# Performance work log

Hardware: AMD Instinct MI355X
Metric: run time of the kernel (lower is better)

## Reference

```python
import jax, jax.numpy as jnp
import numpy as np

B, L, E, H, V, NC = 64, 256, 300, 128, 50000, 2
NH1, F1 = 8, 8  # GAT layer 1: 8 heads x 8 features; layer 2: 1 head x 1 feature
LRELU = 0.2


def _lstm_dir(x, W, U, b):
    # x: [B, L, E]; W: [4H, E]; U: [4H, H]; b: [4H] (b_ih + b_hh fused)
    Bq, Hq = x.shape[0], U.shape[1]
    def step(carry, xt):
        h, c = carry
        g = xt @ W.T + h @ U.T + b
        i, f, gg, o = jnp.split(g, 4, axis=-1)  # PyTorch gate order i,f,g,o
        c = jax.nn.sigmoid(f) * c + jax.nn.sigmoid(i) * jnp.tanh(gg)
        h = jax.nn.sigmoid(o) * jnp.tanh(c)
        return (h, c), h
    h0 = jnp.zeros((Bq, Hq), x.dtype)
    _, hs = jax.lax.scan(step, (h0, h0), jnp.swapaxes(x, 0, 1))
    return jnp.swapaxes(hs, 0, 1)  # [B, L, H]


def bilstm(x, Wf, Uf, bf, Wb, Ub, bb):
    hf = _lstm_dir(x, Wf, Uf, bf)
    hb = _lstm_dir(x[:, ::-1], Wb, Ub, bb)[:, ::-1]
    return jnp.concatenate([hf, hb], axis=-1)  # [B, L, 2H]


def gat_layer(x, W, a_src, a_trg, bias, n_heads, f_out, concat, elu_act):
    # Dense equivalent of GAT IMP3 on a fully-connected graph (edge (s,t): src=s, trg=t).
    Bq, Lq, _ = x.shape
    proj = (x @ W.T).reshape(Bq, Lq, n_heads, f_out)        # [B,L,NH,F]
    s_src = jnp.einsum('blhf,hf->blh', proj, a_src)          # [B,L,NH]
    s_trg = jnp.einsum('blhf,hf->blh', proj, a_trg)
    sc = jax.nn.leaky_relu(s_src[:, :, None, :] + s_trg[:, None, :, :], LRELU)  # [B,S,T,NH]
    m = jnp.max(sc, axis=(1, 2, 3), keepdims=True)           # global max per graph (as in IMP3)
    e = jnp.exp(sc - m)
    A = e / (jnp.sum(e, axis=1, keepdims=True) + 1e-16)      # softmax over sources per target
    out = jnp.einsum('bsth,bshf->bthf', A, proj)             # scatter-aggregate to targets
    if concat:
        out = out.reshape(Bq, Lq, n_heads * f_out)
    else:
        out = out.mean(axis=2)
    out = out + bias
    if elu_act:
        out = jax.nn.elu(out)
    return out, A


def setup_inputs() -> dict:
    key = jax.random.key(0)
    ks = jax.random.split(key, 20)
    n = lambda k, shape, s=0.05: (jax.random.normal(k, shape, jnp.float32) * s)
    return {
        'input_ids': jax.random.randint(ks[0], (B, L), 0, V, jnp.int32),
        'attention_mask': jnp.ones((B, L), bool),
        'emb': n(ks[1], (V, E), 0.1),
        'Wih_f': n(ks[2], (4 * H, E)), 'Whh_f': n(ks[3], (4 * H, H)), 'b_f': jnp.zeros((4 * H,), jnp.float32),
        'Wih_b': n(ks[4], (4 * H, E)), 'Whh_b': n(ks[5], (4 * H, H)), 'b_b': jnp.zeros((4 * H,), jnp.float32),
        'g1_W': n(ks[6], (NH1 * F1, 2 * H)), 'g1_src': n(ks[7], (NH1, F1), 0.1), 'g1_trg': n(ks[8], (NH1, F1), 0.1), 'g1_b': jnp.zeros((NH1 * F1,), jnp.float32),
        'g2_W': n(ks[9], (1, NH1 * F1)), 'g2_src': n(ks[10], (1, 1), 0.1), 'g2_trg': n(ks[11], (1, 1), 0.1), 'g2_b': jnp.zeros((1,), jnp.float32),
        'ctx': n(ks[12], (L, 1), 0.1),
        'lin_W': n(ks[13], (B, 2 * H)), 'lin_b': jnp.zeros((B,), jnp.float32),
        'out_W': n(ks[14], (NC, B)), 'out_b': jnp.zeros((NC,), jnp.float32),
    }


def reference(input_ids, attention_mask, emb, Wih_f, Whh_f, b_f, Wih_b, Whh_b, b_b,
              g1_W, g1_src, g1_trg, g1_b, g2_W, g2_src, g2_trg, g2_b,
              ctx, lin_W, lin_b, out_W, out_b):
    x = emb[input_ids]                                   # [B,L,E] (dropout = eval no-op)
    h_seq = bilstm(x, Wih_f, Whh_f, b_f, Wih_b, Whh_b, b_b)  # [B,L,2H]
    h1, _ = gat_layer(h_seq, g1_W, g1_src, g1_trg, g1_b, NH1, F1, True, True)
    _, A2 = gat_layer(h1, g2_W, g2_src, g2_trg, g2_b, 1, 1, False, False)
    att2 = A2[..., 0]                                    # [B, src, trg] == att.view(-1, 2H) rows
    att = jnp.einsum('bst,t->bs', att2, ctx[:, 0])       # mm with context_vector
    att = jnp.where(attention_mask, att, -jnp.inf)
    att = jax.nn.softmax(att, axis=1)                    # [B,L]
    pooled = jnp.max(h_seq * att[..., None], axis=1)     # [B,2H]
    hcl = jax.nn.relu(pooled @ lin_W.T + lin_b)
    logits = hcl @ out_W.T + out_b                       # [B,NC]
    return (logits, att)
```

## Files before the change

### kernel.cpp

```cpp
#include <hip/hip_runtime.h>
#include <math.h>
#include <stdint.h>

#define Bq 64
#define Lq 256
#define Eq 300
#define Hq 128
#define MQ (Bq*Lq)
#define AST 320

#define LRELU_S 0.2f

__device__ __forceinline__ float lrelu(float x) { return x > 0.f ? x : LRELU_S * x; }

typedef short short8 __attribute__((ext_vector_type(8)));
typedef float f32x4v __attribute__((ext_vector_type(4)));

__device__ __forceinline__ unsigned short f2bf(float x) {
  unsigned u = __float_as_uint(x);
  u += 0x7FFFu + ((u >> 16) & 1u);
  return (unsigned short)(u >> 16);
}
__device__ __forceinline__ float bf2f(unsigned short h) {
  return __uint_as_float(((unsigned)h) << 16);
}

__global__ __launch_bounds__(256) void gather_conv_kernel(
    const float* __restrict__ emb, const int* __restrict__ ids,
    unsigned short* __restrict__ Agh, unsigned short* __restrict__ Agl)
{
  const int JOBS = MQ * 80;
  for (int j = blockIdx.x * blockDim.x + threadIdx.x; j < JOBS;
       j += gridDim.x * blockDim.x) {
    int row = j / 80, c = j - row * 80;
    uint2 ph = make_uint2(0u, 0u), pl = make_uint2(0u, 0u);
    if (c < 75) {
      float4 v = *(const float4*)(emb + (size_t)ids[row] * Eq + c * 4);
      unsigned short h0 = f2bf(v.x), h1 = f2bf(v.y), h2 = f2bf(v.z), h3 = f2bf(v.w);
      unsigned short l0 = f2bf(v.x - bf2f(h0)), l1 = f2bf(v.y - bf2f(h1));
      unsigned short l2 = f2bf(v.z - bf2f(h2)), l3 = f2bf(v.w - bf2f(h3));
      ph.x = (unsigned)h0 | ((unsigned)h1 << 16); ph.y = (unsigned)h2 | ((unsigned)h3 << 16);
      pl.x = (unsigned)l0 | ((unsigned)l1 << 16); pl.y = (unsigned)l2 | ((unsigned)l3 << 16);
    }
    size_t off = (size_t)row * AST + c * 4;
    *(uint2*)(Agh + off) = ph;
    *(uint2*)(Agl + off) = pl;
  }
}

#define BM 64
#define BN 64
#define BK 16

__global__ __launch_bounds__(256) void gemm_awt(
    const float* __restrict__ Asrc, const int* __restrict__ ids,
    const float* __restrict__ W, const float* __restrict__ bias,
    float* __restrict__ C, int M, int N, int K)
{
  __shared__ float As[BK][BM + 4];
  __shared__ float Bs[BK][BN + 4];
  int tid = threadIdx.x;
  int tx = tid & 15, ty = tid >> 4;
  int row0 = blockIdx.x * BM, col0 = blockIdx.y * BN;

  int lrow = tid >> 2;
  int lk   = (tid & 3) << 2;

  const float* Arow;
  {
    int r = row0 + lrow;
    int id = ids ? ids[r] : r;
    Arow = Asrc + (size_t)id * K;
  }
  const float* Wrow = W + (size_t)(col0 + lrow) * K;

  float acc[4][4] = {};

  for (int k0 = 0; k0 < K; k0 += BK) {
    int kk = k0 + lk;
    float4 av, bv;
    if (kk + 3 < K) {
      av = *(const float4*)(Arow + kk);
      bv = *(const float4*)(Wrow + kk);
    } else {
      float a0 = (kk + 0 < K) ? Arow[kk + 0] : 0.f;
      float a1 = (kk + 1 < K) ? Arow[kk + 1] : 0.f;
      float a2 = (kk + 2 < K) ? Arow[kk + 2] : 0.f;
      float a3 = (kk + 3 < K) ? Arow[kk + 3] : 0.f;
      av = make_float4(a0, a1, a2, a3);
      float b0 = (kk + 0 < K) ? Wrow[kk + 0] : 0.f;
      float b1 = (kk + 1 < K) ? Wrow[kk + 1] : 0.f;
      float b2 = (kk + 2 < K) ? Wrow[kk + 2] : 0.f;
      float b3 = (kk + 3 < K) ? Wrow[kk + 3] : 0.f;
      bv = make_float4(b0, b1, b2, b3);
    }
    As[lk + 0][lrow] = av.x; As[lk + 1][lrow] = av.y;
    As[lk + 2][lrow] = av.z; As[lk + 3][lrow] = av.w;
    Bs[lk + 0][lrow] = bv.x; Bs[lk + 1][lrow] = bv.y;
    Bs[lk + 2][lrow] = bv.z; Bs[lk + 3][lrow] = bv.w;
    __syncthreads();

    #pragma unroll
    for (int k = 0; k < BK; ++k) {
      float4 a4 = *(const float4*)&As[k][ty * 4];
      float4 b4 = *(const float4*)&Bs[k][tx * 4];
      float a[4] = {a4.x, a4.y, a4.z, a4.w};
      float bb[4] = {b4.x, b4.y, b4.z, b4.w};
      #pragma unroll
      for (int i = 0; i < 4; ++i)
        #pragma unroll
        for (int j = 0; j < 4; ++j)
          acc[i][j] += a[i] * bb[j];
    }
    __syncthreads();
  }

  #pragma unroll
  for (int i = 0; i < 4; ++i) {
    int r = row0 + ty * 4 + i;
    #pragma unroll
    for (int j = 0; j < 4; ++j) {
      int cidx = col0 + tx * 4 + j;
      float v = acc[i][j] + (bias ? bias[cidx] : 0.f);
      C[(size_t)r * N + cidx] = v;
    }
  }
}

__global__ __launch_bounds__(256) void gemm_gates_mfma(
    const unsigned short* __restrict__ Agh, const unsigned short* __restrict__ Agl,
    const float* __restrict__ Wf, const float* __restrict__ bf,
    const float* __restrict__ Wb, const float* __restrict__ bb_,
    float* __restrict__ C)
{
  __shared__ __align__(16) short Ah[128 * 32];
  __shared__ __align__(16) short Al[128 * 32];
  __shared__ __align__(16) short Bh[128 * 32];
  __shared__ __align__(16) short Bl[128 * 32];

  int tid = threadIdx.x;
  int row0 = blockIdx.x * 128;
  int col0 = blockIdx.y * 128;
  const float* W    = (col0 < 512) ? Wf : Wb;
  const float* bias = (col0 < 512) ? bf : bb_;
  int wcol0 = col0 & 511;

  int l  = tid & 63, wv = tid >> 6;
  int wm = wv >> 1,  wn = wv & 1;
  int kq = l >> 4,   rl = l & 15;

  f32x4v acc[4][4] = {};

  for (int k0 = 0; k0 < 300; k0 += 32) {
    #pragma unroll
    for (int p = 0; p < 4; ++p) {
      int idx = p * 256 + tid;
      int row = idx >> 3, c4 = idx & 7;
      int gk = k0 + c4 * 4;
      int chunk = (c4 >> 1) ^ ((row >> 2) & 3);
      int off = row * 32 + chunk * 8 + (c4 & 1) * 4;
      {
        size_t ao = (size_t)(row0 + row) * AST + gk;
        *(uint2*)&Ah[off] = *(const uint2*)(Agh + ao);
        *(uint2*)&Al[off] = *(const uint2*)(Agl + ao);
      }
      {
        float4 bv = make_float4(0.f, 0.f, 0.f, 0.f);
        if (gk < 300)
          bv = *(const float4*)(W + (size_t)(wcol0 + row) * 300 + gk);
        unsigned short h0 = f2bf(bv.x), h1 = f2bf(bv.y), h2 = f2bf(bv.z), h3 = f2bf(bv.w);
        unsigned short l0 = f2bf(bv.x - bf2f(h0)), l1 = f2bf(bv.y - bf2f(h1));
        unsigned short l2 = f2bf(bv.z - bf2f(h2)), l3 = f2bf(bv.w - bf2f(h3));
        uint2 ph; ph.x = (unsigned)h0 | ((unsigned)h1 << 16); ph.y = (unsigned)h2 | ((unsigned)h3 << 16);
        uint2 pl; pl.x = (unsigned)l0 | ((unsigned)l1 << 16); pl.y = (unsigned)l2 | ((unsigned)l3 << 16);
        *(uint2*)&Bh[off] = ph;
        *(uint2*)&Bl[off] = pl;
      }
    }
    __syncthreads();

    short8 ah[4], al_[4], bh[4], bl[4];
    #pragma unroll
    for (int f = 0; f < 4; ++f) {
      int ar = wm * 64 + f * 16 + rl;
      int ac = kq ^ ((ar >> 2) & 3);
      ah[f]  = *(const short8*)&Ah[ar * 32 + ac * 8];
      al_[f] = *(const short8*)&Al[ar * 32 + ac * 8];
      int br = wn * 64 + f * 16 + rl;
      int bc = kq ^ ((br >> 2) & 3);
      bh[f]  = *(const short8*)&Bh[br * 32 + bc * 8];
      bl[f]  = *(const short8*)&Bl[br * 32 + bc * 8];
    }
    #pragma unroll
    for (int fm = 0; fm < 4; ++fm)
      #pragma unroll
      for (int fn = 0; fn < 4; ++fn) {
        acc[fm][fn] = __builtin_amdgcn_mfma_f32_16x16x32_bf16(ah[fm],  bh[fn], acc[fm][fn], 0, 0, 0);
        acc[fm][fn] = __builtin_amdgcn_mfma_f32_16x16x32_bf16(ah[fm],  bl[fn], acc[fm][fn], 0, 0, 0);
        acc[fm][fn] = __builtin_amdgcn_mfma_f32_16x16x32_bf16(al_[fm], bh[fn], acc[fm][fn], 0, 0, 0);
      }
    __syncthreads();
  }

  int fq = l >> 4;
  #pragma unroll
  for (int fm = 0; fm < 4; ++fm) {
    #pragma unroll
    for (int fn = 0; fn < 4; ++fn) {
      int gr = row0 + wm * 64 + fm * 16 + fq * 4;
      int lc = wn * 64 + fn * 16 + rl;
      float bsv = bias[wcol0 + lc];
      #pragma unroll
      for (int i = 0; i < 4; ++i)
        C[(size_t)(gr + i) * 1024 + col0 + lc] = acc[fm][fn][i] + bsv;
    }
  }
}

#define MVB(s0,s1,s2,s3, u0,u1,u2,u3, off) \
  "s_waitcnt lgkmcnt(5)\n" \
  "v_fmac_f32 v88, v" #s0 ", v" #u0 "\n" \
  "v_fmac_f32 v89, v" #s1 ", v" #u1 "\n" \
  "v_fmac_f32 v90, v" #s2 ", v" #u2 "\n" \
  "v_fmac_f32 v91, v" #s3 ", v" #u3 "\n" \
  "ds_read_b128 v[" #s0 ":" #s3 "], v81 offset:" #off "\n"

#define MVT(n, s0,s1,s2,s3, u0,u1,u2,u3) \
  "s_waitcnt lgkmcnt(" #n ")\n" \
  "v_fmac_f32 v88, v" #s0 ", v" #u0 "\n" \
  "v_fmac_f32 v89, v" #s1 ", v" #u1 "\n" \
  "v_fmac_f32 v90, v" #s2 ", v" #u2 "\n" \
  "v_fmac_f32 v91, v" #s3 ", v" #u3 "\n"

#define ULD(lo,hi,off) \
  "global_load_dwordx4 v[" #lo ":" #hi "], v80, %[ub] offset:" #off "\n"

__global__ __launch_bounds__(512, 1) void lstm_kernel(
    const float* __restrict__ ws_base,
    const float* __restrict__ Uf, const float* __restrict__ Ub,
    float* __restrict__ h_seq)
{
  __shared__ __align__(1024) float h_sh[2][Hq];
  int blk = blockIdx.x;
  int b = blk & 63;
  int dir = blk >> 6;
  int j = threadIdx.x;
  int lane = j & 63;
  int w = j >> 6;
  int gate = (lane >> 4) & 3;
  int hidx = (w << 4) | (lane & 15);
  int row = (gate << 7) | hidx;

  const float* U = dir ? Ub : Uf;
  int tt0 = dir ? (Lq - 1) : 0;

  unsigned uo  = (unsigned)row * (Hq * 4u);
  unsigned go0 = (1024u + (unsigned)(b * Lq + tt0) * 1024u
                  + (unsigned)dir * 512u + (unsigned)row) * 4u;
  unsigned ho0 = ((unsigned)(b * Lq + tt0) * 256u
                  + (unsigned)dir * (unsigned)Hq + (unsigned)hidx) * 4u;
  int gd = dir ? -4096 : 4096;
  int hd = dir ? -1024 : 1024;

  unsigned lds_base = (unsigned)(uintptr_t)&h_sh[0][0];
  unsigned ldsr0 = lds_base;
  unsigned ldsw0 = lds_base + 512u + (unsigned)hidx * 4u;

  bool isg = (gate == 2);
  float klog = isg ? -2.8853900817779268f : -1.4426950408889634f;
  float mc = isg ? 2.f : 1.f;
  float ac = isg ? -1.f : 0.f;
  int base4 = (lane & 15) * 4;
  int bp0 = base4, bp1 = base4 + 64, bp2 = base4 + 128, bp3 = base4 + 192;

  if (j < Hq) h_sh[0][j] = 0.f;
  __syncthreads();

  asm volatile(
    "v_mov_b32 v80, %[uo]\n"
    "v_mov_b32 v81, %[ldsr0]\n"
    "v_mov_b32 v82, %[ldsw0]\n"
    "v_mov_b32 v83, %[go0]\n"
    "v_mov_b32 v84, %[ho0]\n"
    "v_mov_b32 v87, 0\n"
    "s_mov_b32 s90, 0\n"
    ULD(128,131,0)   ULD(132,135,16)  ULD(136,139,32)  ULD(140,143,48)
    ULD(144,147,64)  ULD(148,151,80)  ULD(152,155,96)  ULD(156,159,112)
    ULD(160,163,128) ULD(164,167,144) ULD(168,171,160) ULD(172,175,176)
    ULD(176,179,192) ULD(180,183,208) ULD(184,187,224) ULD(188,191,240)
    ULD(192,195,256) ULD(196,199,272) ULD(200,203,288) ULD(204,207,304)
    ULD(208,211,320) ULD(212,215,336) ULD(216,219,352) ULD(220,223,368)
    ULD(224,227,384) ULD(228,231,400) ULD(232,235,416) ULD(236,239,432)
    ULD(240,243,448) ULD(244,247,464) ULD(248,251,480) ULD(252,255,496)
    "global_load_dword v85, v83, %[wsb]\n"
    "s_waitcnt vmcnt(0)\n"
    "Ltop_%=:\n"
    "v_add_u32 v83, %[gd], v83\n"
    "global_load_dword v86, v83, %[wsb]\n"
    "ds_read_b128 v[100:103], v81\n"
    "ds_read_b128 v[104:107], v81 offset:16\n"
    "ds_read_b128 v[108:111], v81 offset:32\n"
    "ds_read_b128 v[112:115], v81 offset:48\n"
    "ds_read_b128 v[116:119], v81 offset:64\n"
    "ds_read_b128 v[120:123], v81 offset:80\n"
    "v_mov_b32 v88, v85\n"
    "v_mov_b32 v89, 0\n"
    "v_mov_b32 v90, 0\n"
    "v_mov_b32 v91, 0\n"
    MVB(100,101,102,103, 128,129,130,131, 96)
    MVB(104,105,106,107, 132,133,134,135, 112)
    MVB(108,109,110,111, 136,137,138,139, 128)
    MVB(112,113,114,115, 140,141,142,143, 144)
    MVB(116,117,118,119, 144,145,146,147, 160)
    MVB(120,121,122,123, 148,149,150,151, 176)
    MVB(100,101,102,103, 152,153,154,155, 192)
    MVB(104,105,106,107, 156,157,158,159, 208)
    MVB(108,109,110,111, 160,161,162,163, 224)
    MVB(112,113,114,115, 164,165,166,167, 240)
    MVB(116,117,118,119, 168,169,170,171, 256)
    MVB(120,121,122,123, 172,173,174,175, 272)
    MVB(100,101,102,103, 176,177,178,179, 288)
    MVB(104,105,106,107, 180,181,182,183, 304)
    MVB(108,109,110,111, 184,185,186,187, 320)
    MVB(112,113,114,115, 188,189,190,191, 336)
    MVB(116,117,118,119, 192,193,194,195, 352)
    MVB(120,121,122,123, 196,197,198,199, 368)
    MVB(100,101,102,103, 200,201,202,203, 384)
    MVB(104,105,106,107, 204,205,206,207, 400)
    MVB(108,109,110,111, 208,209,210,211, 416)
    MVB(112,113,114,115, 212,213,214,215, 432)
    MVB(116,117,118,119, 216,217,218,219, 448)
    MVB(120,121,122,123, 220,221,222,223, 464)
    MVB(100,101,102,103, 224,225,226,227, 480)
    MVB(104,105,106,107, 228,229,230,231, 496)
    MVT(5, 108,109,110,111, 232,233,234,235)
    MVT(4, 112,113,114,115, 236,237,238,239)
    MVT(3, 116,117,118,119, 240,241,242,243)
    MVT(2, 120,121,122,123, 244,245,246,247)
    MVT(1, 100,101,102,103, 248,249,250,251)
    MVT(0, 104,105,106,107, 252,253,254,255)
    "v_add_f32 v88, v88, v90\n"
    "v_add_f32 v89, v89, v91\n"
    "v_add_f32 v88, v88, v89\n"
    "v_mul_f32 v92, %[klog], v88\n"
    "v_exp_f32 v93, v92\n"
    "s_nop 1\n"
    "v_add_f32 v94, 1.0, v93\n"
    "v_rcp_f32 v95, v94\n"
    "s_nop 1\n"
    "v_fma_f32 v97, v95, %[mc], %[ac]\n"
    "ds_bpermute_b32 v92, %[bp0], v97\n"
    "ds_bpermute_b32 v93, %[bp1], v97\n"
    "ds_bpermute_b32 v94, %[bp2], v97\n"
    "ds_bpermute_b32 v98, %[bp3], v97\n"
    "s_waitcnt lgkmcnt(0)\n"
    "v_mul_f32 v95, v92, v94\n"
    "v_fma_f32 v87, v93, v87, v95\n"
    "v_mul_f32 v92, 0xc038aa3b, v87\n"
    "v_exp_f32 v93, v92\n"
    "s_nop 1\n"
    "v_add_f32 v94, 1.0, v93\n"
    "v_rcp_f32 v95, v94\n"
    "s_nop 1\n"
    "v_fma_f32 v96, v95, 2.0, -1.0\n"
    "v_mul_f32 v96, v98, v96\n"
    "s_waitcnt vmcnt(0)\n"
    "v_mov_b32 v85, v86\n"
    "ds_write_b32 v82, v96\n"
    "global_store_dword v84, v96, %[hsb]\n"
    "v_add_u32 v84, %[hd], v84\n"
    "v_xor_b32 v81, 0x200, v81\n"
    "v_xor_b32 v82, 0x200, v82\n"
    "s_waitcnt lgkmcnt(0)\n"
    "s_barrier\n"
    "s_add_u32 s90, s90, 1\n"
    "s_cmp_lt_u32 s90, 256\n"
    "s_cbranch_scc1 Ltop_%=\n"
    "s_waitcnt vmcnt(0) lgkmcnt(0)\n"
    :
    : [wsb]"s"(ws_base), [hsb]"s"(h_seq), [ub]"s"(U),
      [gd]"s"(gd), [hd]"s"(hd),
      [uo]"v"(uo), [go0]"v"(go0), [ho0]"v"(ho0),
      [ldsr0]"v"(ldsr0), [ldsw0]"v"(ldsw0),
      [klog]"v"(klog), [mc]"v"(mc), [ac]"v"(ac),
      [bp0]"v"(bp0), [bp1]"v"(bp1), [bp2]"v"(bp2), [bp3]"v"(bp3)
    : "memory", "scc", "s90",
      "v80","v81","v82","v83","v84","v85","v86","v87","v88","v89",
      "v90","v91","v92","v93","v94","v95","v96","v97","v98",
      "v100","v101","v102","v103","v104","v105","v106","v107",
      "v108","v109","v110","v111","v112","v113","v114","v115",
      "v116","v117","v118","v119","v120","v121","v122","v123",
      "v128","v129","v130","v131","v132","v133","v134","v135",
      "v136","v137","v138","v139","v140","v141","v142","v143",
      "v144","v145","v146","v147","v148","v149","v150","v151",
      "v152","v153","v154","v155","v156","v157","v158","v159",
      "v160","v161","v162","v163","v164","v165","v166","v167",
      "v168","v169","v170","v171","v172","v173","v174","v175",
      "v176","v177","v178","v179","v180","v181","v182","v183",
      "v184","v185","v186","v187","v188","v189","v190","v191",
      "v192","v193","v194","v195","v196","v197","v198","v199",
      "v200","v201","v202","v203","v204","v205","v206","v207",
      "v208","v209","v210","v211","v212","v213","v214","v215",
      "v216","v217","v218","v219","v220","v221","v222","v223",
      "v224","v225","v226","v227","v228","v229","v230","v231",
      "v232","v233","v234","v235","v236","v237","v238","v239",
      "v240","v241","v242","v243","v244","v245","v246","v247",
      "v248","v249","v250","v251","v252","v253","v254","v255");
}
#undef MVB
#undef MVT
#undef ULD

__device__ __forceinline__ float block_max_256(float v, volatile float* red) {
  #pragma unroll
  for (int o = 32; o > 0; o >>= 1) v = fmaxf(v, __shfl_xor(v, o, 64));
  int tid = threadIdx.x;
  if ((tid & 63) == 0) red[tid >> 6] = v;
  __syncthreads();
  float r = fmaxf(fmaxf(red[0], red[1]), fmaxf(red[2], red[3]));
  __syncthreads();
  return r;
}
__device__ __forceinline__ float block_sum_256(float v, volatile float* red) {
  #pragma unroll
  for (int o = 32; o > 0; o >>= 1) v += __shfl_xor(v, o, 64);
  int tid = threadIdx.x;
  if ((tid & 63) == 0) red[tid >> 6] = v;
  __syncthreads();
  float r = red[0] + red[1] + red[2] + red[3];
  __syncthreads();
  return r;
}

__global__ __launch_bounds__(256) void gat1_fused_kernel(
    const float* __restrict__ proj1, const float* __restrict__ g1_src,
    const float* __restrict__ g1_trg, const float* __restrict__ g1_b,
    float* __restrict__ h1)
{
  int b = blockIdx.x >> 3;
  int h = blockIdx.x & 7;
  int t = threadIdx.x;
  __shared__ float src_s[Lq], trg_s[Lq];
  __shared__ float proj_s[Lq * 8];
  __shared__ float red[4];

  size_t base = (size_t)b * Lq;
  float pv[8];
  {
    const float4* pr = (const float4*)(proj1 + (base + t) * 64 + h * 8);
    float4 p0 = pr[0], p1 = pr[1];
    pv[0]=p0.x; pv[1]=p0.y; pv[2]=p0.z; pv[3]=p0.w;
    pv[4]=p1.x; pv[5]=p1.y; pv[6]=p1.z; pv[7]=p1.w;
    float4* psh = (float4*)(proj_s + t * 8);
    psh[0] = p0; psh[1] = p1;
  }
  float ss = 0.f, st = 0.f;
  #pragma unroll
  for (int f = 0; f < 8; ++f) {
    ss += pv[f] * g1_src[h * 8 + f];
    st += pv[f] * g1_trg[h * 8 + f];
  }
  src_s[t] = ss;
  trg_s[t] = st;
  __syncthreads();

  float ms = block_max_256(ss, red);
  float mt = block_max_256(st, red);
  float m = lrelu(ms + mt);

  float mytrg = trg_s[t];
  float den = 1e-16f;
  float acc[8] = {};
  for (int s = 0; s < Lq; ++s) {
    float wgt = __expf(lrelu(src_s[s] + mytrg) - m);
    den += wgt;
    const float* ps = proj_s + s * 8;
    #pragma unroll
    for (int f = 0; f < 8; ++f) acc[f] += wgt * ps[f];
  }
  float inv = 1.f / den;
  float* out = h1 + (base + t) * 64 + h * 8;
  #pragma unroll
  for (int f = 0; f < 8; ++f) {
    float v = acc[f] * inv + g1_b[h * 8 + f];
    out[f] = v > 0.f ? v : expm1f(v);
  }
}

__global__ __launch_bounds__(256) void gat2_pool_head_kernel(
    const float* __restrict__ h1, const float* __restrict__ g2_W,
    const float* __restrict__ g2_src, const float* __restrict__ g2_trg,
    const float* __restrict__ ctx, const float* __restrict__ h_seq,
    const float* __restrict__ lin_W, const float* __restrict__ lin_b,
    const float* __restrict__ out_W, const float* __restrict__ out_b,
    float* __restrict__ att_out, float* __restrict__ logits)
{
  int b = blockIdx.x;
  int tid = threadIdx.x;
  __shared__ float w2[64];
  __shared__ float src2[Lq], trg2[Lq], dq[Lq], att_sh[Lq], pool_sh[256];
  __shared__ float red[4];
  __shared__ float part[4][64];
  __shared__ float hcl[64];

  if (tid < 64) w2[tid] = g2_W[tid];
  __syncthreads();

  const float* hr = h1 + ((size_t)b * Lq + tid) * 64;
  float p = 0.f;
  #pragma unroll
  for (int k = 0; k < 64; ++k) p += hr[k] * w2[k];
  float a_s = g2_src[0], a_t = g2_trg[0];
  src2[tid] = p * a_s;
  trg2[tid] = p * a_t;
  __syncthreads();

  float ms = block_max_256(src2[tid], red);
  float mt = block_max_256(trg2[tid], red);
  float m2 = lrelu(ms + mt);

  float mytrg = trg2[tid];
  float d0 = 1e-16f, d1 = 0.f, d2 = 0.f, d3 = 0.f;
  for (int s = 0; s < Lq; s += 4) {
    d0 += __expf(lrelu(src2[s + 0] + mytrg) - m2);
    d1 += __expf(lrelu(src2[s + 1] + mytrg) - m2);
    d2 += __expf(lrelu(src2[s + 2] + mytrg) - m2);
    d3 += __expf(lrelu(src2[s + 3] + mytrg) - m2);
  }
  dq[tid] = ctx[tid] / ((d0 + d1) + (d2 + d3));
  __syncthreads();

  float mysrc = src2[tid];
  float r0 = 0.f, r1 = 0.f, r2 = 0.f, r3 = 0.f;
  for (int t = 0; t < Lq; t += 4) {
    r0 += dq[t + 0] * __expf(lrelu(mysrc + trg2[t + 0]) - m2);
    r1 += dq[t + 1] * __expf(lrelu(mysrc + trg2[t + 1]) - m2);
    r2 += dq[t + 2] * __expf(lrelu(mysrc + trg2[t + 2]) - m2);
    r3 += dq[t + 3] * __expf(lrelu(mysrc + trg2[t + 3]) - m2);
  }
  float raw = (r0 + r1) + (r2 + r3);

  float mr = block_max_256(raw, red);
  float e = __expf(raw - mr);
  float ssum = block_sum_256(e, red);
  float att = e / ssum;
  att_out[(size_t)b * Lq + tid] = att;
  att_sh[tid] = att;
  __syncthreads();

  float pm = -3.4e38f;
  const float* hb = h_seq + (size_t)b * Lq * 256 + tid;
  for (int l = 0; l < Lq; l += 4) {
    float v0 = hb[(size_t)(l + 0) * 256] * att_sh[l + 0];
    float v1 = hb[(size_t)(l + 1) * 256] * att_sh[l + 1];
    float v2 = hb[(size_t)(l + 2) * 256] * att_sh[l + 2];
    float v3 = hb[(size_t)(l + 3) * 256] * att_sh[l + 3];
    pm = fmaxf(pm, fmaxf(fmaxf(v0, v1), fmaxf(v2, v3)));
  }
  pool_sh[tid] = pm;
  __syncthreads();

  {
    int jj = tid & 63, kq = tid >> 6;
    const float* pr = pool_sh + kq * 64;
    const float* wr = lin_W + jj * 256 + kq * 64;
    float d = 0.f;
    #pragma unroll
    for (int k = 0; k < 64; ++k) d += pr[k] * wr[k];
    part[kq][jj] = d;
  }
  __syncthreads();
  if (tid < 64) {
    float v = part[0][tid] + part[1][tid] + part[2][tid] + part[3][tid] + lin_b[tid];
    hcl[tid] = fmaxf(v, 0.f);
  }
  __syncthreads();
  if (tid < 128) {
    int cc = tid >> 6, jj = tid & 63;
    float pp = hcl[jj] * out_W[cc * 64 + jj];
    #pragma unroll
    for (int o = 32; o > 0; o >>= 1) pp += __shfl_xor(pp, o, 64);
    if (jj == 0) logits[b * 2 + cc] = pp + out_b[cc];
  }
}

extern "C" void kernel_launch(void* const* d_in, const int* in_sizes, int n_in,
                              void* d_out, int out_size, void* d_ws, size_t ws_size,
                              hipStream_t stream)
{
  const int*   ids    = (const int*)  d_in[0];
  const float* emb    = (const float*)d_in[2];
  const float* Wih_f  = (const float*)d_in[3];
  const float* Whh_f  = (const float*)d_in[4];
  const float* b_f    = (const float*)d_in[5];
  const float* Wih_b  = (const float*)d_in[6];
  const float* Whh_b  = (const float*)d_in[7];
  const float* b_b    = (const float*)d_in[8];
  const float* g1_W   = (const float*)d_in[9];
  const float* g1_src = (const float*)d_in[10];
  const float* g1_trg = (const float*)d_in[11];
  const float* g1_b   = (const float*)d_in[12];
  const float* g2_W   = (const float*)d_in[13];
  const float* g2_src = (const float*)d_in[14];
  const float* g2_trg = (const float*)d_in[15];
  const float* ctx    = (const float*)d_in[17];
  const float* lin_W  = (const float*)d_in[18];
  const float* lin_b  = (const float*)d_in[19];
  const float* out_W  = (const float*)d_in[20];
  const float* out_b  = (const float*)d_in[21];

  float* out_f   = (float*)d_out;
  float* logits  = out_f;
  float* att_out = out_f + 128;

  float* ws = (float*)d_ws;
  const size_t M = MQ;
  float* ws_base = ws;
  ws += 1024;
  float* gates   = ws; ws += M * 1024;
  float* h_seq   = ws; ws += M * 256;
  float* proj1   = ws; ws += M * 64;
  float* h1      = ws; ws += M * 64;
  unsigned short* Agh = (unsigned short*)ws; ws += M * AST / 2;
  unsigned short* Agl = (unsigned short*)ws; ws += M * AST / 2;

  dim3 thr(256);

  gather_conv_kernel<<<2048, thr, 0, stream>>>(emb, ids, Agh, Agl);

  gemm_gates_mfma<<<dim3(MQ / 128, 1024 / 128), thr, 0, stream>>>(Agh, Agl, Wih_f, b_f, Wih_b, b_b, gates);

  lstm_kernel<<<128, 512, 0, stream>>>(ws_base, Whh_f, Whh_b, h_seq);

  gemm_awt<<<dim3(MQ / BM, 1), thr, 0, stream>>>(h_seq, nullptr, g1_W, nullptr, proj1, MQ, 64, 256);
  gat1_fused_kernel<<<Bq * 8, thr, 0, stream>>>(proj1, g1_src, g1_trg, g1_b, h1);

  gat2_pool_head_kernel<<<Bq, thr, 0, stream>>>(h1, g2_W, g2_src, g2_trg, ctx, h_seq,
                                                lin_W, lin_b, out_W, out_b,
                                                att_out, logits);
}
```

Baseline: 328.5 us.

## Pre-split weights to bf16 pairs once and use MFMA for GAT projection

Input-projection weights and the GAT1 weight are converted once into bf16 hi/lo pairs by a new kernel, so the gates GEMM no longer redoes that split in every tile. The LSTM kernel now also writes its hidden states as bf16 hi/lo pairs. A new split-bf16 MFMA GEMM uses these for the GAT1 projection, replacing the scalar fp32 tiled GEMM. The cost is an extra launch, more workspace, and two extra stores per step in the latency-bound LSTM loop.

```diff
diff --git a/kernel.cpp b/kernel.cpp
--- a/kernel.cpp
+++ b/kernel.cpp
@@ -25,6 +25,16 @@
   return __uint_as_float(((unsigned)h) << 16);
 }
 
+__device__ __forceinline__ void cv4(float4 v, unsigned short* dh, unsigned short* dl) {
+  unsigned short h0 = f2bf(v.x), h1 = f2bf(v.y), h2 = f2bf(v.z), h3 = f2bf(v.w);
+  unsigned short l0 = f2bf(v.x - bf2f(h0)), l1 = f2bf(v.y - bf2f(h1));
+  unsigned short l2 = f2bf(v.z - bf2f(h2)), l3 = f2bf(v.w - bf2f(h3));
+  uint2 ph; ph.x = (unsigned)h0 | ((unsigned)h1 << 16); ph.y = (unsigned)h2 | ((unsigned)h3 << 16);
+  uint2 pl; pl.x = (unsigned)l0 | ((unsigned)l1 << 16); pl.y = (unsigned)l2 | ((unsigned)l3 << 16);
+  *(uint2*)dh = ph;
+  *(uint2*)dl = pl;
+}
+
 __global__ __launch_bounds__(256) void gather_conv_kernel(
     const float* __restrict__ emb, const int* __restrict__ ids,
     unsigned short* __restrict__ Agh, unsigned short* __restrict__ Agl)
@@ -33,104 +43,53 @@
   for (int j = blockIdx.x * blockDim.x + threadIdx.x; j < JOBS;
        j += gridDim.x * blockDim.x) {
     int row = j / 80, c = j - row * 80;
-    uint2 ph = make_uint2(0u, 0u), pl = make_uint2(0u, 0u);
+    size_t off = (size_t)row * AST + c * 4;
     if (c < 75) {
       float4 v = *(const float4*)(emb + (size_t)ids[row] * Eq + c * 4);
-      unsigned short h0 = f2bf(v.x), h1 = f2bf(v.y), h2 = f2bf(v.z), h3 = f2bf(v.w);
-      unsigned short l0 = f2bf(v.x - bf2f(h0)), l1 = f2bf(v.y - bf2f(h1));
-      unsigned short l2 = f2bf(v.z - bf2f(h2)), l3 = f2bf(v.w - bf2f(h3));
-      ph.x = (unsigned)h0 | ((unsigned)h1 << 16); ph.y = (unsigned)h2 | ((unsigned)h3 << 16);
-      pl.x = (unsigned)l0 | ((unsigned)l1 << 16); pl.y = (unsigned)l2 | ((unsigned)l3 << 16);
-    }
-    size_t off = (size_t)row * AST + c * 4;
-    *(uint2*)(Agh + off) = ph;
-    *(uint2*)(Agl + off) = pl;
-  }
-}
-
-#define BM 64
-#define BN 64
-#define BK 16
-
-__global__ __launch_bounds__(256) void gemm_awt(
-    const float* __restrict__ Asrc, const int* __restrict__ ids,
-    const float* __restrict__ W, const float* __restrict__ bias,
-    float* __restrict__ C, int M, int N, int K)
-{
-  __shared__ float As[BK][BM + 4];
-  __shared__ float Bs[BK][BN + 4];
-  int tid = threadIdx.x;
-  int tx = tid & 15, ty = tid >> 4;
-  int row0 = blockIdx.x * BM, col0 = blockIdx.y * BN;
-
-  int lrow = tid >> 2;
-  int lk   = (tid & 3) << 2;
-
-  const float* Arow;
-  {
-    int r = row0 + lrow;
-    int id = ids ? ids[r] : r;
-    Arow = Asrc + (size_t)id * K;
-  }
-  const float* Wrow = W + (size_t)(col0 + lrow) * K;
-
-  float acc[4][4] = {};
-
-  for (int k0 = 0; k0 < K; k0 += BK) {
-    int kk = k0 + lk;
-    float4 av, bv;
-    if (kk + 3 < K) {
-      av = *(const float4*)(Arow + kk);
-      bv = *(const float4*)(Wrow + kk);
+      cv4(v, Agh + off, Agl + off);
     } else {
-      float a0 = (kk + 0 < K) ? Arow[kk + 0] : 0.f;
-      float a1 = (kk + 1 < K) ? Arow[kk + 1] : 0.f;
-      float a2 = (kk + 2 < K) ? Arow[kk + 2] : 0.f;
-      float a3 = (kk + 3 < K) ? Arow[kk + 3] : 0.f;
-      av = make_float4(a0, a1, a2, a3);
-      float b0 = (kk + 0 < K) ? Wrow[kk + 0] : 0.f;
-      float b1 = (kk + 1 < K) ? Wrow[kk + 1] : 0.f;
-      float b2 = (kk + 2 < K) ? Wrow[kk + 2] : 0.f;
-      float b3 = (kk + 3 < K) ? Wrow[kk + 3] : 0.f;
-      bv = make_float4(b0, b1, b2, b3);
-    }
-    As[lk + 0][lrow] = av.x; As[lk + 1][lrow] = av.y;
-    As[lk + 2][lrow] = av.z; As[lk + 3][lrow] = av.w;
-    Bs[lk + 0][lrow] = bv.x; Bs[lk + 1][lrow] = bv.y;
-    Bs[lk + 2][lrow] = bv.z; Bs[lk + 3][lrow] = bv.w;
-    __syncthreads();
-
-    #pragma unroll
-    for (int k = 0; k < BK; ++k) {
-      float4 a4 = *(const float4*)&As[k][ty * 4];
-      float4 b4 = *(const float4*)&Bs[k][tx * 4];
-      float a[4] = {a4.x, a4.y, a4.z, a4.w};
-      float bb[4] = {b4.x, b4.y, b4.z, b4.w};
-      #pragma unroll
-      for (int i = 0; i < 4; ++i)
-        #pragma unroll
-        for (int j = 0; j < 4; ++j)
-          acc[i][j] += a[i] * bb[j];
-    }
-    __syncthreads();
-  }
-
-  #pragma unroll
-  for (int i = 0; i < 4; ++i) {
-    int r = row0 + ty * 4 + i;
-    #pragma unroll
-    for (int j = 0; j < 4; ++j) {
-      int cidx = col0 + tx * 4 + j;
-      float v = acc[i][j] + (bias ? bias[cidx] : 0.f);
-      C[(size_t)r * N + cidx] = v;
+      *(uint2*)(Agh + off) = make_uint2(0u, 0u);
+      *(uint2*)(Agl + off) = make_uint2(0u, 0u);
+    }
+  }
+}
+
+__global__ __launch_bounds__(256) void conv_w_kernel(
+    const float* __restrict__ Wf, const float* __restrict__ Wb,
+    const float* __restrict__ g1_W,
+    unsigned short* __restrict__ Wbh, unsigned short* __restrict__ Wbl,
+    unsigned short* __restrict__ g1h, unsigned short* __restrict__ g1l)
+{
+  const int J1 = 1024 * 80;
+  const int J2 = 64 * 64;
+  for (int j = blockIdx.x * blockDim.x + threadIdx.x; j < J1 + J2;
+       j += gridDim.x * blockDim.x) {
+    if (j < J1) {
+      int row = j / 80, c = j - row * 80;
+      size_t off = (size_t)row * AST + c * 4;
+      if (c < 75) {
+        const float* src = (row < 512) ? (Wf + (size_t)row * 300)
+                                       : (Wb + (size_t)(row - 512) * 300);
+        float4 v = *(const float4*)(src + c * 4);
+        cv4(v, Wbh + off, Wbl + off);
+      } else {
+        *(uint2*)(Wbh + off) = make_uint2(0u, 0u);
+        *(uint2*)(Wbl + off) = make_uint2(0u, 0u);
+      }
+    } else {
+      int j2 = j - J1;
+      int row = j2 >> 6, c = j2 & 63;
+      size_t off = (size_t)row * 256 + c * 4;
+      float4 v = *(const float4*)(g1_W + off);
+      cv4(v, g1h + off, g1l + off);
     }
   }
 }
 
 __global__ __launch_bounds__(256) void gemm_gates_mfma(
     const unsigned short* __restrict__ Agh, const unsigned short* __restrict__ Agl,
-    const float* __restrict__ Wf, const float* __restrict__ bf,
-    const float* __restrict__ Wb, const float* __restrict__ bb_,
+    const unsigned short* __restrict__ Wbh, const unsigned short* __restrict__ Wbl,
+    const float* __restrict__ bf, const float* __restrict__ bb_,
     float* __restrict__ C)
 {
   __shared__ __align__(16) short Ah[128 * 32];
@@ -141,7 +100,6 @@
   int tid = threadIdx.x;
   int row0 = blockIdx.x * 128;
   int col0 = blockIdx.y * 128;
-  const float* W    = (col0 < 512) ? Wf : Wb;
   const float* bias = (col0 < 512) ? bf : bb_;
   int wcol0 = col0 & 511;
 
@@ -159,23 +117,12 @@
       int gk = k0 + c4 * 4;
       int chunk = (c4 >> 1) ^ ((row >> 2) & 3);
       int off = row * 32 + chunk * 8 + (c4 & 1) * 4;
-      {
-        size_t ao = (size_t)(row0 + row) * AST + gk;
-        *(uint2*)&Ah[off] = *(const uint2*)(Agh + ao);
-        *(uint2*)&Al[off] = *(const uint2*)(Agl + ao);
-      }
-      {
-        float4 bv = make_float4(0.f, 0.f, 0.f, 0.f);
-        if (gk < 300)
-          bv = *(const float4*)(W + (size_t)(wcol0 + row) * 300 + gk);
-        unsigned short h0 = f2bf(bv.x), h1 = f2bf(bv.y), h2 = f2bf(bv.z), h3 = f2bf(bv.w);
-        unsigned short l0 = f2bf(bv.x - bf2f(h0)), l1 = f2bf(bv.y - bf2f(h1));
-        unsigned short l2 = f2bf(bv.z - bf2f(h2)), l3 = f2bf(bv.w - bf2f(h3));
-        uint2 ph; ph.x = (unsigned)h0 | ((unsigned)h1 << 16); ph.y = (unsigned)h2 | ((unsigned)h3 << 16);
-        uint2 pl; pl.x = (unsigned)l0 | ((unsigned)l1 << 16); pl.y = (unsigned)l2 | ((unsigned)l3 << 16);
-        *(uint2*)&Bh[off] = ph;
-        *(uint2*)&Bl[off] = pl;
-      }
+      size_t ao = (size_t)(row0 + row) * AST + gk;
+      *(uint2*)&Ah[off] = *(const uint2*)(Agh + ao);
+      *(uint2*)&Al[off] = *(const uint2*)(Agl + ao);
+      size_t bo = (size_t)(col0 + row) * AST + gk;
+      *(uint2*)&Bh[off] = *(const uint2*)(Wbh + bo);
+      *(uint2*)&Bl[off] = *(const uint2*)(Wbl + bo);
     }
     __syncthreads();
 
@@ -217,6 +164,90 @@
   }
 }
 
+__global__ __launch_bounds__(256) void gemm_proj_mfma(
+    const unsigned short* __restrict__ Hbh, const unsigned short* __restrict__ Hbl,
+    const unsigned short* __restrict__ g1h, const unsigned short* __restrict__ g1l,
+    float* __restrict__ C)
+{
+  __shared__ __align__(16) short Ah[128 * 32];
+  __shared__ __align__(16) short Al[128 * 32];
+  __shared__ __align__(16) short Bh[64 * 32];
+  __shared__ __align__(16) short Bl[64 * 32];
+
+  int tid = threadIdx.x;
+  int row0 = blockIdx.x * 128;
+
+  int l  = tid & 63, wv = tid >> 6;
+  int wm = wv >> 1,  wn = wv & 1;
+  int kq = l >> 4,   rl = l & 15;
+
+  f32x4v acc[4][2] = {};
+
+  for (int k0 = 0; k0 < 256; k0 += 32) {
+    #pragma unroll
+    for (int p = 0; p < 4; ++p) {
+      int idx = p * 256 + tid;
+      int row = idx >> 3, c4 = idx & 7;
+      int gk = k0 + c4 * 4;
+      int chunk = (c4 >> 1) ^ ((row >> 2) & 3);
+      int off = row * 32 + chunk * 8 + (c4 & 1) * 4;
+      size_t ao = (size_t)(row0 + row) * 256 + gk;
+      *(uint2*)&Ah[off] = *(const uint2*)(Hbh + ao);
+      *(uint2*)&Al[off] = *(const uint2*)(Hbl + ao);
+    }
+    #pragma unroll
+    for (int p = 0; p < 2; ++p) {
+      int idx = p * 256 + tid;
+      int row = idx >> 3, c4 = idx & 7;
+      int gk = k0 + c4 * 4;
+      int chunk = (c4 >> 1) ^ ((row >> 2) & 3);
+      int off = row * 32 + chunk * 8 + (c4 & 1) * 4;
+      size_t bo = (size_t)row * 256 + gk;
+      *(uint2*)&Bh[off] = *(const uint2*)(g1h + bo);
+      *(uint2*)&Bl[off] = *(const uint2*)(g1l + bo);
+    }
+    __syncthreads();
+
+    short8 ah[4], al_[4], bh[2], bl[2];
+    #pragma unroll
+    for (int f = 0; f < 4; ++f) {
+      int ar = wm * 64 + f * 16 + rl;
+      int ac = kq ^ ((ar >> 2) & 3);
+      ah[f]  = *(const short8*)&Ah[ar * 32 + ac * 8];
+      al_[f] = *(const short8*)&Al[ar * 32 + ac * 8];
+    }
+    #pragma unroll
+    for (int f = 0; f < 2; ++f) {
+      int br = wn * 32 + f * 16 + rl;
+      int bc = kq ^ ((br >> 2) & 3);
+      bh[f]  = *(const short8*)&Bh[br * 32 + bc * 8];
+      bl[f]  = *(const short8*)&Bl[br * 32 + bc * 8];
+    }
+    #pragma unroll
+    for (int fm = 0; fm < 4; ++fm)
+      #pragma unroll
+      for (int fn = 0; fn < 2; ++fn) {
+        acc[fm][fn] = __builtin_amdgcn_mfma_f32_16x16x32_bf16(ah[fm],  bh[fn], acc[fm][fn], 0, 0, 0);
+        acc[fm][fn] = __builtin_amdgcn_mfma_f32_16x16x32_bf16(ah[fm],  bl[fn], acc[fm][fn], 0, 0, 0);
+        acc[fm][fn] = __builtin_amdgcn_mfma_f32_16x16x32_bf16(al_[fm], bh[fn], acc[fm][fn], 0, 0, 0);
+      }
+    __syncthreads();
+  }
+
+  int fq = l >> 4;
+  #pragma unroll
+  for (int fm = 0; fm < 4; ++fm) {
+    #pragma unroll
+    for (int fn = 0; fn < 2; ++fn) {
+      int gr = row0 + wm * 64 + fm * 16 + fq * 4;
+      int lc = wn * 32 + fn * 16 + rl;
+      #pragma unroll
+      for (int i = 0; i < 4; ++i)
+        C[(size_t)(gr + i) * 64 + lc] = acc[fm][fn][i];
+    }
+  }
+}
+
 #define MVB(s0,s1,s2,s3, u0,u1,u2,u3, off) \
   "s_waitcnt lgkmcnt(5)\n" \
   "v_fmac_f32 v88, v" #s0 ", v" #u0 "\n" \
@@ -238,7 +269,8 @@
 __global__ __launch_bounds__(512, 1) void lstm_kernel(
     const float* __restrict__ ws_base,
     const float* __restrict__ Uf, const float* __restrict__ Ub,
-    float* __restrict__ h_seq)
+    float* __restrict__ h_seq,
+    unsigned short* __restrict__ Hbh, unsigned short* __restrict__ Hbl)
 {
   __shared__ __align__(1024) float h_sh[2][Hq];
   int blk = blockIdx.x;
@@ -259,8 +291,11 @@
                   + (unsigned)dir * 512u + (unsigned)row) * 4u;
   unsigned ho0 = ((unsigned)(b * Lq + tt0) * 256u
                   + (unsigned)dir * (unsigned)Hq + (unsigned)hidx) * 4u;
-  int gd = dir ? -4096 : 4096;
-  int hd = dir ? -1024 : 1024;
+  unsigned hb0 = ((unsigned)(b * Lq + tt0) * 256u
+                  + (unsigned)dir * (unsigned)Hq + (unsigned)hidx) * 2u;
+  int gd  = dir ? -4096 : 4096;
+  int hd  = dir ? -1024 : 1024;
+  int hdb = dir ? -512  : 512;
 
   unsigned lds_base = (unsigned)(uintptr_t)&h_sh[0][0];
   unsigned ldsr0 = lds_base;
@@ -282,6 +317,7 @@
     "v_mov_b32 v82, %[ldsw0]\n"
     "v_mov_b32 v83, %[go0]\n"
     "v_mov_b32 v84, %[ho0]\n"
+    "v_mov_b32 v74, %[hb0]\n"
     "v_mov_b32 v87, 0\n"
     "s_mov_b32 s90, 0\n"
     ULD(128,131,0)   ULD(132,135,16)  ULD(136,139,32)  ULD(140,143,48)
@@ -364,11 +400,24 @@
     "s_nop 1\n"
     "v_fma_f32 v96, v95, 2.0, -1.0\n"
     "v_mul_f32 v96, v98, v96\n"
+    "v_bfe_u32 v75, v96, 16, 1\n"
+    "v_add_u32 v75, 0x7fff, v75\n"
+    "v_add_u32 v76, v96, v75\n"
+    "v_lshrrev_b32 v77, 16, v76\n"
+    "v_lshlrev_b32 v78, 16, v77\n"
+    "v_sub_f32 v78, v96, v78\n"
+    "v_bfe_u32 v75, v78, 16, 1\n"
+    "v_add_u32 v75, 0x7fff, v75\n"
+    "v_add_u32 v79, v78, v75\n"
+    "v_lshrrev_b32 v79, 16, v79\n"
     "s_waitcnt vmcnt(0)\n"
     "v_mov_b32 v85, v86\n"
     "ds_write_b32 v82, v96\n"
     "global_store_dword v84, v96, %[hsb]\n"
+    "global_store_short v74, v77, %[hbh]\n"
+    "global_store_short v74, v79, %[hbl]\n"
     "v_add_u32 v84, %[hd], v84\n"
+    "v_add_u32 v74, %[hdb], v74\n"
     "v_xor_b32 v81, 0x200, v81\n"
     "v_xor_b32 v82, 0x200, v82\n"
     "s_waitcnt lgkmcnt(0)\n"
@@ -379,12 +428,14 @@
     "s_waitcnt vmcnt(0) lgkmcnt(0)\n"
     :
     : [wsb]"s"(ws_base), [hsb]"s"(h_seq), [ub]"s"(U),
-      [gd]"s"(gd), [hd]"s"(hd),
-      [uo]"v"(uo), [go0]"v"(go0), [ho0]"v"(ho0),
+      [hbh]"s"(Hbh), [hbl]"s"(Hbl),
+      [gd]"s"(gd), [hd]"s"(hd), [hdb]"s"(hdb),
+      [uo]"v"(uo), [go0]"v"(go0), [ho0]"v"(ho0), [hb0]"v"(hb0),
       [ldsr0]"v"(ldsr0), [ldsw0]"v"(ldsw0),
       [klog]"v"(klog), [mc]"v"(mc), [ac]"v"(ac),
       [bp0]"v"(bp0), [bp1]"v"(bp1), [bp2]"v"(bp2), [bp3]"v"(bp3)
     : "memory", "scc", "s90",
+      "v74","v75","v76","v77","v78","v79",
       "v80","v81","v82","v83","v84","v85","v86","v87","v88","v89",
       "v90","v91","v92","v93","v94","v95","v96","v97","v98",
       "v100","v101","v102","v103","v104","v105","v106","v107",
@@ -623,16 +674,23 @@
   float* h1      = ws; ws += M * 64;
   unsigned short* Agh = (unsigned short*)ws; ws += M * AST / 2;
   unsigned short* Agl = (unsigned short*)ws; ws += M * AST / 2;
+  unsigned short* Wbh = (unsigned short*)ws; ws += 1024 * AST / 2;
+  unsigned short* Wbl = (unsigned short*)ws; ws += 1024 * AST / 2;
+  unsigned short* g1h = (unsigned short*)ws; ws += 64 * 256 / 2;
+  unsigned short* g1l = (unsigned short*)ws; ws += 64 * 256 / 2;
+  unsigned short* Hbh = (unsigned short*)ws; ws += M * 256 / 2;
+  unsigned short* Hbl = (unsigned short*)ws; ws += M * 256 / 2;
 
   dim3 thr(256);
 
   gather_conv_kernel<<<2048, thr, 0, stream>>>(emb, ids, Agh, Agl);
-
-  gemm_gates_mfma<<<dim3(MQ / 128, 1024 / 128), thr, 0, stream>>>(Agh, Agl, Wih_f, b_f, Wih_b, b_b, gates);
-
-  lstm_kernel<<<128, 512, 0, stream>>>(ws_base, Whh_f, Whh_b, h_seq);
-
-  gemm_awt<<<dim3(MQ / BM, 1), thr, 0, stream>>>(h_seq, nullptr, g1_W, nullptr, proj1, MQ, 64, 256);
+  conv_w_kernel<<<512, thr, 0, stream>>>(Wih_f, Wih_b, g1_W, Wbh, Wbl, g1h, g1l);
+
+  gemm_gates_mfma<<<dim3(MQ / 128, 1024 / 128), thr, 0, stream>>>(Agh, Agl, Wbh, Wbl, b_f, b_b, gates);
+
+  lstm_kernel<<<128, 512, 0, stream>>>(ws_base, Whh_f, Whh_b, h_seq, Hbh, Hbl);
+
+  gemm_proj_mfma<<<MQ / 128, thr, 0, stream>>>(Hbh, Hbl, g1h, g1l, proj1);
   gat1_fused_kernel<<<Bq * 8, thr, 0, stream>>>(proj1, g1_src, g1_trg, g1_b, h1);
 
   gat2_pool_head_kernel<<<Bq, thr, 0, stream>>>(h1, g2_W, g2_src, g2_trg, ctx, h_seq,
```

Measured after the change: 307.8 us. 1.07x faster.
